# Optimization experiments

Measured on AMD Instinct MI355X. Metric: run time of the kernel, lower is better.

## Reference

```python
import jax, jax.numpy as jnp
import numpy as np

NUM_NODES = 256
IN_FEAT = 64
HIDDEN = 512
N_CLASSES = 2
BATCH = 256


def setup_inputs() -> dict:
    key = jax.random.key(0)
    ks = jax.random.split(key, 10)
    return {
        "z": jax.random.normal(ks[0], (BATCH, 1, NUM_NODES, NUM_NODES), dtype=jnp.float32),
        "node_emb": jax.random.normal(ks[1], (NUM_NODES, IN_FEAT), dtype=jnp.float32),
        "w1": jax.random.normal(ks[2], (IN_FEAT, HIDDEN), dtype=jnp.float32) * (1.0 / np.sqrt(IN_FEAT)),
        "b1": jnp.zeros((HIDDEN,), dtype=jnp.float32),
        "w2": jax.random.normal(ks[3], (HIDDEN, HIDDEN), dtype=jnp.float32) * (1.0 / np.sqrt(HIDDEN)),
        "b2": jnp.zeros((HIDDEN,), dtype=jnp.float32),
        "w3": jax.random.normal(ks[4], (HIDDEN, HIDDEN), dtype=jnp.float32) * (1.0 / np.sqrt(HIDDEN)),
        "b3": jnp.zeros((HIDDEN,), dtype=jnp.float32),
        "fcw": jax.random.normal(ks[5], (HIDDEN, N_CLASSES), dtype=jnp.float32) * (1.0 / np.sqrt(HIDDEN)),
        "fcb": jnp.zeros((N_CLASSES,), dtype=jnp.float32),
    }


def reference(z, node_emb, w1, b1, w2, b2, w3, b3, fcw, fcb):
    # z: (B, 1, N, N) latent interpreted as weighted adjacency
    z_sq = jnp.squeeze(z, axis=1)                         # (B, N, N)
    A = jax.nn.sigmoid(z_sq)
    A = (A + jnp.swapaxes(A, 1, 2)) * 0.5                  # symmetrize
    A_hat = A + jnp.eye(A.shape[-1], dtype=A.dtype)[None]  # add self loops
    D_hat = jnp.sum(A_hat, axis=2) + 1e-6                  # (B, N) degrees
    d_inv_sqrt = D_hat ** -0.5
    # norm_A = D^{-1/2} A_hat D^{-1/2} via row/col scaling (same math as diag bmm)
    norm_A = A_hat * d_inv_sqrt[:, :, None] * d_inv_sqrt[:, None, :]

    X = jnp.broadcast_to(node_emb[None], (z.shape[0],) + node_emb.shape)  # (B, N, F)
    H1 = jax.nn.relu(jnp.einsum('bij,bjh->bih', norm_A, X @ w1 + b1))
    H2 = jax.nn.relu(jnp.einsum('bij,bjh->bih', norm_A, H1 @ w2 + b2))
    H3 = jax.nn.relu(jnp.einsum('bij,bjh->bih', norm_A, H2 @ w3 + b3))
    graph_emb = jnp.mean(H3, axis=1)                       # (B, H)
    logits = graph_emb @ fcw + fcb                         # (B, n_classes)
    return logits
```

## Files before the change

### kernel.cpp

```cpp
#include <hip/hip_runtime.h>
#include <stdint.h>

#define B_ 256
#define N_ 256
#define F_ 64
#define H_ 512

typedef _Float16 f16;
typedef _Float16 f16x8 __attribute__((ext_vector_type(8)));
typedef _Float16 f16x4 __attribute__((ext_vector_type(4)));
typedef _Float16 f16x2 __attribute__((ext_vector_type(2)));
typedef float    f32x4 __attribute__((ext_vector_type(4)));

__device__ __forceinline__ float sigmoidf_(float x) {
    return 1.0f / (1.0f + __expf(-x));
}

#define BAR_ACQ(N) do { \
    asm volatile("s_waitcnt vmcnt(" #N ")" ::: "memory"); \
    __builtin_amdgcn_s_barrier(); \
    __builtin_amdgcn_sched_barrier(0); } while (0)
#define BAR_REL() do { \
    __builtin_amdgcn_sched_barrier(0); \
    __builtin_amdgcn_s_barrier(); } while (0)

__global__ __launch_bounds__(512) void k_fsum(const float* __restrict__ z,
                                              f16* __restrict__ nA) {
    constexpr int LD = 258;
    __shared__ f16 T[256 * LD];
    __shared__ float cpart[8][256];
    __shared__ float rbuf[256];
    __shared__ float Dv[256];

    const int b = blockIdx.x;
    const int tid = threadIdx.x, lane = tid & 63, w = tid >> 6;
    const float* zb = z + (size_t)b * (N_ * N_);

    float colacc[4] = {0.f, 0.f, 0.f, 0.f};
    for (int r = 0; r < 32; r++) {
        int i = w * 32 + r;
        float4 v = *(const float4*)(zb + (size_t)i * N_ + lane * 4);
        float s0 = sigmoidf_(v.x), s1 = sigmoidf_(v.y),
              s2 = sigmoidf_(v.z), s3 = sigmoidf_(v.w);
        f16x2 p0 = { (f16)s0, (f16)s1 }, p1 = { (f16)s2, (f16)s3 };
        *(f16x2*)&T[i * LD + lane * 4]     = p0;
        *(f16x2*)&T[i * LD + lane * 4 + 2] = p1;
        colacc[0] += s0; colacc[1] += s1; colacc[2] += s2; colacc[3] += s3;
        float rs = s0 + s1 + s2 + s3;
        for (int off = 32; off; off >>= 1) rs += __shfl_down(rs, off, 64);
        if (lane == 0) rbuf[i] = rs;
    }
    #pragma unroll
    for (int k = 0; k < 4; k++) cpart[w][lane * 4 + k] = colacc[k];
    __syncthreads();

    if (tid < 256) {
        float cs = 0.f;
        #pragma unroll
        for (int ww = 0; ww < 8; ww++) cs += cpart[ww][tid];
        Dv[tid] = rsqrtf(1.0f + 1e-6f + 0.5f * (rbuf[tid] + cs));
    }
    __syncthreads();

    const int j8 = (tid & 31) * 8;
    float dj[8];
    #pragma unroll
    for (int k = 0; k < 8; k++) dj[k] = Dv[j8 + k];
    f16* Ob = nA + (size_t)b * (N_ * N_);
    for (int it = 0; it < 16; it++) {
        int i = it * 16 + (tid >> 5);
        float di = Dv[i];
        f16x2 dd[4];
        #pragma unroll
        for (int c = 0; c < 4; c++)
            dd[c] = *(const f16x2*)&T[i * LD + j8 + c * 2];
        f16x8 o;
        #pragma unroll
        for (int k = 0; k < 8; k++) {
            float sij = (float)dd[k >> 1][k & 1];
            float v = 0.5f * (sij + (float)T[(j8 + k) * LD + i]);
            if (i == j8 + k) v += 1.0f;
            o[k] = (f16)(v * di * dj[k]);
        }
        *(f16x8*)&Ob[(size_t)i * N_ + j8] = o;
    }
}

__global__ __launch_bounds__(256) void k_prep(const float* __restrict__ ne,
                                              const float* __restrict__ w1,
                                              const float* __restrict__ b1,
                                              const float* __restrict__ w2,
                                              const float* __restrict__ w3,
                                              f16* __restrict__ XW1t,
                                              f16* __restrict__ w2t,
                                              f16* __restrict__ w3t) {
    int bid = blockIdx.x;
    if (bid < 512) {
        int h = bid, node = threadIdx.x;
        float s = b1[h];
        #pragma unroll 8
        for (int k = 0; k < F_; k++) s += ne[node * F_ + k] * w1[k * H_ + h];
        XW1t[h * N_ + node] = (f16)s;
    } else {
        int idx4 = bid - 512;
        int which = idx4 >> 10;
        const float* src = which ? w3 : w2;
        f16* dst = which ? w3t : w2t;
        int idx = (idx4 & 1023) * 256 + threadIdx.x;
        int k = idx >> 9, n = idx & 511;
        dst[n * H_ + k] = (f16)src[k * H_ + n];
    }
}

template <int KDIM, int MODE>
__global__ __launch_bounds__(256, 4) void k_gemm(const f16* __restrict__ A, long aBatch,
                                                 const f16* __restrict__ Bt, long bBatch,
                                                 f16* __restrict__ Out,
                                                 const float* __restrict__ bias,
                                                 float* __restrict__ gp) {
    __shared__ f16 As[128 * 64];
    __shared__ f16 Bs[128 * 64];
    const int tid  = threadIdx.x;
    const int lane = tid & 63, wave = tid >> 6;
    const int wm = wave >> 1, wn = wave & 1;

    const int lin = blockIdx.x;
    const int xcd = lin & 7, q = lin >> 3;
    const int n_t = q & 3, p = q >> 2;
    const int grp = xcd * 64 + p;
    const int b   = grp >> 1, m_t = grp & 1;
    const int m0 = m_t * 128, n0 = n_t * 128;

    const f16* Ab = A + (size_t)b * aBatch;
    const f16* Bb = Bt + (size_t)b * bBatch;

    f32x4 acc[4][4];
    #pragma unroll
    for (int i = 0; i < 4; i++)
        #pragma unroll
        for (int j = 0; j < 4; j++)
            #pragma unroll
            for (int r = 0; r < 4; r++) acc[i][j][r] = 0.0f;

    const int lr = lane >> 3;
    const int kc = (lane & 7) ^ lr;

    const int ln15 = lane & 15;

    for (int kk = 0; kk < KDIM; kk += 64) {
        #pragma unroll
        for (int c = 0; c < 4; c++) {
            int chunk = wave * 4 + c;
            int row = chunk * 8 + lr;
            __builtin_amdgcn_global_load_lds(
                (__attribute__((address_space(1))) void*)(Ab + (size_t)(m0 + row) * KDIM + kk + kc * 8),
                (__attribute__((address_space(3))) void*)(&As[chunk * 512]), 16, 0, 0);
            __builtin_amdgcn_global_load_lds(
                (__attribute__((address_space(1))) void*)(Bb + (size_t)(n0 + row) * KDIM + kk + kc * 8),
                (__attribute__((address_space(3))) void*)(&Bs[chunk * 512]), 16, 0, 0);
        }
        __syncthreads();

        #pragma unroll
        for (int ks = 0; ks < 2; ks++) {
            const int rkc = ks * 4 + (lane >> 4);
            f16x8 aF[4];
            #pragma unroll
            for (int t = 0; t < 4; t++) {
                int ra = wm * 64 + t * 16 + ln15;
                aF[t] = *(const f16x8*)&As[(ra * 8 + (rkc ^ (ra & 7))) * 8];
            }
            #pragma unroll
            for (int h2 = 0; h2 < 2; h2++) {
                f16x8 bF[2];
                #pragma unroll
                for (int t = 0; t < 2; t++) {
                    int rb = wn * 64 + (h2 * 2 + t) * 16 + ln15;
                    bF[t] = *(const f16x8*)&Bs[(rb * 8 + (rkc ^ (rb & 7))) * 8];
                }
                #pragma unroll
                for (int mt = 0; mt < 4; mt++)
                    #pragma unroll
                    for (int t = 0; t < 2; t++)
                        acc[mt][h2 * 2 + t] = __builtin_amdgcn_mfma_f32_16x16x32_f16(aF[mt], bF[t], acc[mt][h2 * 2 + t], 0, 0, 0);
            }
        }
        __syncthreads();
    }

    const int quad = lane >> 4;
    if (MODE == 0) {
        f16* Ob = Out + (size_t)b * (N_ * H_);
        #pragma unroll
        for (int mt = 0; mt < 4; mt++) {
            int node = m0 + wm * 64 + mt * 16 + quad * 4;
            #pragma unroll
            for (int nt = 0; nt < 4; nt++) {
                int h = n0 + wn * 64 + nt * 16 + ln15;
                #pragma unroll
                for (int rr = 0; rr < 4; rr++) {
                    float v = acc[mt][nt][rr];
                    v = v > 0.f ? v : 0.f;
                    Ob[(size_t)(node + rr) * H_ + h] = (f16)v;
                }
            }
        }
    }
}

template <int REDUCE>
__global__ __launch_bounds__(512, 2) void k_fused(const f16* __restrict__ Hin,
                                                  const f16* __restrict__ Wt,
                                                  const float* __restrict__ bias,
                                                  const f16* __restrict__ nA,
                                                  f16* __restrict__ Hout,
                                                  float* __restrict__ gp) {
    __shared__ f16 As[2][16384];
    __shared__ f16 WU[32768];

    const int tid  = threadIdx.x;
    const int lane = tid & 63, wave = tid >> 6;
    const int ln15 = lane & 15, quad = lane >> 4;
    const int wm = wave >> 1, wn = wave & 1;

    const int lin = blockIdx.x;
    const int xcd = lin & 7, p = lin >> 3;
    const int grp = xcd * 128 + p;
    const int b = grp >> 2, hc = grp & 3;

    const f16* Hb = Hin + (size_t)b * (N_ * H_);
    const f16* Ab = nA + (size_t)b * (N_ * N_);
    const f16* Wc = Wt + (size_t)(hc * 128) * H_;

    const int lr = lane >> 3;
    const int kc = (lane & 7) ^ lr;

    auto stage1 = [&](int buf, int kt) {
        #pragma unroll
        for (int c = 0; c < 4; c++) {
            int chunk = wave * 4 + c;
            int row = chunk * 8 + lr;
            __builtin_amdgcn_global_load_lds(
                (__attribute__((address_space(1))) void*)(Hb + (size_t)row * H_ + kt * 64 + kc * 8),
                (__attribute__((address_space(3))) void*)(&As[buf][chunk * 512]), 16, 0, 0);
        }
        #pragma unroll
        for (int c = 0; c < 2; c++) {
            int chunk = wave * 2 + c;
            int row = chunk * 8 + lr;
            __builtin_amdgcn_global_load_lds(
                (__attribute__((address_space(1))) void*)(Wc + (size_t)row * H_ + kt * 64 + kc * 8),
                (__attribute__((address_space(3))) void*)(&WU[buf * 8192 + chunk * 512]), 16, 0, 0);
        }
    };
    auto stage2 = [&](int buf, int jt) {
        #pragma unroll
        for (int c = 0; c < 4; c++) {
            int chunk = wave * 4 + c;
            int row = chunk * 8 + lr;
            __builtin_amdgcn_global_load_lds(
                (__attribute__((address_space(1))) void*)(Ab + (size_t)row * N_ + jt * 64 + kc * 8),
                (__attribute__((address_space(3))) void*)(&As[buf][chunk * 512]), 16, 0, 0);
        }
    };

    f32x4 acc[4][4];
    #pragma unroll
    for (int i = 0; i < 4; i++)
        #pragma unroll
        for (int j = 0; j < 4; j++)
            #pragma unroll
            for (int r = 0; r < 4; r++) acc[i][j][r] = 0.0f;

    stage1(0, 0);
    for (int kt = 0; kt < 8; ++kt) {
        const int buf = kt & 1;
        if (kt < 7) {
            stage1(buf ^ 1, kt + 1);
            BAR_ACQ(6);
        } else {
            stage2(0, 0);
            BAR_ACQ(4);
        }
        __builtin_amdgcn_s_setprio(1);
        #pragma unroll
        for (int ks = 0; ks < 2; ks++) {
            const int rkc = ks * 4 + quad;
            f16x8 aF[4], bF[4];
            #pragma unroll
            for (int t = 0; t < 4; t++) {
                int ra = wm * 64 + t * 16 + ln15;
                aF[t] = *(const f16x8*)&As[buf][(ra * 8 + (rkc ^ (ra & 7))) * 8];
            }
            #pragma unroll
            for (int t = 0; t < 4; t++) {
                int rb = wn * 64 + t * 16 + ln15;
                bF[t] = *(const f16x8*)&WU[buf * 8192 + (rb * 8 + (rkc ^ (rb & 7))) * 8];
            }
            #pragma unroll
            for (int mt = 0; mt < 4; mt++)
                #pragma unroll
                for (int nt = 0; nt < 4; nt++)
                    acc[mt][nt] = __builtin_amdgcn_mfma_f32_16x16x32_f16(aF[mt], bF[nt], acc[mt][nt], 0, 0, 0);
        }
        __builtin_amdgcn_s_setprio(0);
        BAR_REL();
    }

    #pragma unroll
    for (int nt = 0; nt < 4; nt++) {
        int hl = wn * 64 + nt * 16 + ln15;
        float bv = bias[hc * 128 + hl];
        #pragma unroll
        for (int mt = 0; mt < 4; mt++) {
            int j = wm * 64 + mt * 16 + quad * 4;
            int slot = (j >> 3) ^ (hl & 7);
            f16x4 v;
            #pragma unroll
            for (int rr = 0; rr < 4; rr++) v[rr] = (f16)(acc[mt][nt][rr] + bv);
            *(f16x4*)&WU[hl * 256 + slot * 8 + (j & 7)] = v;
        }
    }
    asm volatile("s_waitcnt lgkmcnt(0)" ::: "memory");
    __builtin_amdgcn_s_barrier();
    __builtin_amdgcn_sched_barrier(0);

    #pragma unroll
    for (int i = 0; i < 4; i++)
        #pragma unroll
        for (int j = 0; j < 4; j++)
            #pragma unroll
            for (int r = 0; r < 4; r++) acc[i][j][r] = 0.0f;

    for (int jt = 0; jt < 4; ++jt) {
        const int buf = jt & 1;
        if (jt < 3) {
            stage2(buf ^ 1, jt + 1);
            BAR_ACQ(4);
        } else {
            BAR_ACQ(0);
        }
        __builtin_amdgcn_s_setprio(1);
        #pragma unroll
        for (int ks = 0; ks < 2; ks++) {
            const int rkc = ks * 4 + quad;
            f16x8 aF[4], bF[4];
            #pragma unroll
            for (int t = 0; t < 4; t++) {
                int ra = wm * 64 + t * 16 + ln15;
                aF[t] = *(const f16x8*)&As[buf][(ra * 8 + (rkc ^ (ra & 7))) * 8];
            }
            #pragma unroll
            for (int t = 0; t < 4; t++) {
                int rb = wn * 64 + t * 16 + ln15;
                int g = jt * 8 + rkc;
                bF[t] = *(const f16x8*)&WU[rb * 256 + ((g ^ (rb & 7)) * 8)];
            }
            #pragma unroll
            for (int mt = 0; mt < 4; mt++)
                #pragma unroll
                for (int nt = 0; nt < 4; nt++)
                    acc[mt][nt] = __builtin_amdgcn_mfma_f32_16x16x32_f16(aF[mt], bF[nt], acc[mt][nt], 0, 0, 0);
        }
        __builtin_amdgcn_s_setprio(0);
        BAR_REL();
    }

    if (REDUCE == 0) {
        f16* Ob = Hout + (size_t)b * (N_ * H_);
        #pragma unroll
        for (int mt = 0; mt < 4; mt++) {
            int node = wm * 64 + mt * 16 + quad * 4;
            #pragma unroll
            for (int nt = 0; nt < 4; nt++) {
                int hg = hc * 128 + wn * 64 + nt * 16 + ln15;
                #pragma unroll
                for (int rr = 0; rr < 4; rr++) {
                    float v = acc[mt][nt][rr];
                    v = v > 0.f ? v : 0.f;
                    Ob[(size_t)(node + rr) * H_ + hg] = (f16)v;
                }
            }
        }
    } else {
        float part[4];
        #pragma unroll
        for (int nt = 0; nt < 4; nt++) {
            float s = 0.f;
            #pragma unroll
            for (int mt = 0; mt < 4; mt++)
                #pragma unroll
                for (int rr = 0; rr < 4; rr++) {
                    float v = acc[mt][nt][rr];
                    s += (v > 0.f ? v : 0.f);
                }
            s += __shfl_down(s, 32, 64);
            s += __shfl_down(s, 16, 64);
            part[nt] = s;
        }
        __syncthreads();
        float* red = (float*)&As[0][0];
        if (quad == 0) {
            #pragma unroll
            for (int nt = 0; nt < 4; nt++)
                red[wave * 64 + nt * 16 + ln15] = part[nt];
        }
        __syncthreads();
        if (tid < 128) {
            int wnl = tid >> 6, cl = tid & 63;
            float g = red[(0 * 2 + wnl) * 64 + cl] + red[(1 * 2 + wnl) * 64 + cl]
                    + red[(2 * 2 + wnl) * 64 + cl] + red[(3 * 2 + wnl) * 64 + cl];
            gp[(size_t)b * H_ + hc * 128 + tid] = g;
        }
    }
}

__global__ __launch_bounds__(256) void k_logits(const float* __restrict__ gp,
                                                const float* __restrict__ fcw,
                                                const float* __restrict__ fcb,
                                                float* __restrict__ out) {
    int b = blockIdx.x, tid = threadIdx.x;
    const float* g = gp + (size_t)b * H_;
    float g0 = g[tid];
    float g1 = g[tid + 256];
    float p0 = g0 * fcw[tid * 2 + 0] + g1 * fcw[(tid + 256) * 2 + 0];
    float p1 = g0 * fcw[tid * 2 + 1] + g1 * fcw[(tid + 256) * 2 + 1];
    for (int off = 32; off; off >>= 1) {
        p0 += __shfl_down(p0, off, 64);
        p1 += __shfl_down(p1, off, 64);
    }
    __shared__ float r0[4], r1[4];
    int lane = tid & 63, w = tid >> 6;
    if (lane == 0) { r0[w] = p0; r1[w] = p1; }
    __syncthreads();
    const float inv = 1.0f / N_;
    if (tid == 0) out[b * 2 + 0] = (r0[0] + r0[1] + r0[2] + r0[3]) * inv + fcb[0];
    if (tid == 1) out[b * 2 + 1] = (r1[0] + r1[1] + r1[2] + r1[3]) * inv + fcb[1];
}

extern "C" void kernel_launch(void* const* d_in, const int* in_sizes, int n_in,
                              void* d_out, int out_size, void* d_ws, size_t ws_size,
                              hipStream_t stream) {
    const float* z   = (const float*)d_in[0];
    const float* ne  = (const float*)d_in[1];
    const float* w1  = (const float*)d_in[2];
    const float* b1  = (const float*)d_in[3];
    const float* w2  = (const float*)d_in[4];
    const float* b2  = (const float*)d_in[5];
    const float* w3  = (const float*)d_in[6];
    const float* b3  = (const float*)d_in[7];
    const float* fcw = (const float*)d_in[8];
    const float* fcb = (const float*)d_in[9];
    float* out = (float*)d_out;

    char* ws = (char*)d_ws;
    f16*   T     = (f16*)(ws + 0);
    f16*   nA    = (f16*)(ws + 67108864);
    f16*   Hh    = (f16*)(ws + 100663296);
    float* gpart = (float*)(ws + 100663296);
    f16*   XW1t  = (f16*)(ws + 167772160);
    f16*   w2t   = (f16*)(ws + 168034304);
    f16*   w3t   = (f16*)(ws + 168558592);

    k_fsum<<<256, 512, 0, stream>>>(z, nA);
    k_prep<<<2560, 256, 0, stream>>>(ne, w1, b1, w2, w3, XW1t, w2t, w3t);

    k_gemm<256, 0><<<2048, 256, 0, stream>>>(nA, 65536, XW1t, 0, Hh, nullptr, nullptr);
    k_fused<0><<<1024, 512, 0, stream>>>(Hh, w2t, b2, nA, T, nullptr);
    k_fused<1><<<1024, 512, 0, stream>>>(T, w3t, b3, nA, nullptr, gpart);

    k_logits<<<B_, 256, 0, stream>>>(gpart, fcw, fcb, out);
}
```

Baseline: 308.0 us.

## Swizzle shared sigmoid tile and symmetrize via 8x8 register tiles

Replaces the padded LDS tile with an XOR-swizzled 256x256 half layout written in 8-byte chunks. The symmetrize/normalize pass now loads 8x8 blocks of rows and columns as vector reads and transposes them in registers, instead of doing scalar strided transposed reads. Row sums move from per-row wave shuffles to a separate LDS pass after the barrier. This is meant to cut LDS bank conflicts and the count of LDS instructions in the adjacency-normalization kernel, in exchange for more register pressure and an extra barrier.

```diff
diff --git a/kernel.cpp b/kernel.cpp
--- a/kernel.cpp
+++ b/kernel.cpp
@@ -26,63 +26,86 @@
 
 __global__ __launch_bounds__(512) void k_fsum(const float* __restrict__ z,
                                               f16* __restrict__ nA) {
-    constexpr int LD = 258;
-    __shared__ f16 T[256 * LD];
+    __shared__ f16 T[256 * 256];
     __shared__ float cpart[8][256];
-    __shared__ float rbuf[256];
+    __shared__ float rpart[256][2];
     __shared__ float Dv[256];
 
     const int b = blockIdx.x;
     const int tid = threadIdx.x, lane = tid & 63, w = tid >> 6;
     const float* zb = z + (size_t)b * (N_ * N_);
 
+    auto swz = [](int i) { return (i & 31) ^ (i >> 5); };
+
     float colacc[4] = {0.f, 0.f, 0.f, 0.f};
+    const int ch = lane >> 1, half = lane & 1;
     for (int r = 0; r < 32; r++) {
         int i = w * 32 + r;
         float4 v = *(const float4*)(zb + (size_t)i * N_ + lane * 4);
         float s0 = sigmoidf_(v.x), s1 = sigmoidf_(v.y),
               s2 = sigmoidf_(v.z), s3 = sigmoidf_(v.w);
-        f16x2 p0 = { (f16)s0, (f16)s1 }, p1 = { (f16)s2, (f16)s3 };
-        *(f16x2*)&T[i * LD + lane * 4]     = p0;
-        *(f16x2*)&T[i * LD + lane * 4 + 2] = p1;
+        f16x4 sv = { (f16)s0, (f16)s1, (f16)s2, (f16)s3 };
+        *(f16x4*)&T[i * 256 + ((ch ^ swz(i)) << 3) + half * 4] = sv;
         colacc[0] += s0; colacc[1] += s1; colacc[2] += s2; colacc[3] += s3;
-        float rs = s0 + s1 + s2 + s3;
-        for (int off = 32; off; off >>= 1) rs += __shfl_down(rs, off, 64);
-        if (lane == 0) rbuf[i] = rs;
     }
     #pragma unroll
     for (int k = 0; k < 4; k++) cpart[w][lane * 4 + k] = colacc[k];
     __syncthreads();
 
+    {
+        int i = tid >> 1, h = tid & 1;
+        float s = 0.f;
+        #pragma unroll
+        for (int c = 0; c < 16; c++) {
+            int cc = h * 16 + c;
+            f16x8 v = *(const f16x8*)&T[i * 256 + ((cc ^ swz(i)) << 3)];
+            #pragma unroll
+            for (int k = 0; k < 8; k++) s += (float)v[k];
+        }
+        rpart[i][h] = s;
+    }
+    __syncthreads();
+
     if (tid < 256) {
         float cs = 0.f;
         #pragma unroll
         for (int ww = 0; ww < 8; ww++) cs += cpart[ww][tid];
-        Dv[tid] = rsqrtf(1.0f + 1e-6f + 0.5f * (rbuf[tid] + cs));
+        float rs = rpart[tid][0] + rpart[tid][1];
+        Dv[tid] = rsqrtf(1.0f + 1e-6f + 0.5f * (rs + cs));
     }
     __syncthreads();
 
-    const int j8 = (tid & 31) * 8;
-    float dj[8];
-    #pragma unroll
-    for (int k = 0; k < 8; k++) dj[k] = Dv[j8 + k];
     f16* Ob = nA + (size_t)b * (N_ * N_);
-    for (int it = 0; it < 16; it++) {
-        int i = it * 16 + (tid >> 5);
-        float di = Dv[i];
-        f16x2 dd[4];
-        #pragma unroll
-        for (int c = 0; c < 4; c++)
-            dd[c] = *(const f16x2*)&T[i * LD + j8 + c * 2];
-        f16x8 o;
-        #pragma unroll
-        for (int k = 0; k < 8; k++) {
-            float sij = (float)dd[k >> 1][k & 1];
-            float v = 0.5f * (sij + (float)T[(j8 + k) * LD + i]);
-            if (i == j8 + k) v += 1.0f;
-            o[k] = (f16)(v * di * dj[k]);
-        }
-        *(f16x8*)&Ob[(size_t)i * N_ + j8] = o;
+    #pragma unroll
+    for (int tt = 0; tt < 2; tt++) {
+        int tile = tt * 512 + tid;
+        int I = tile >> 5, J = tile & 31;
+        f16x8 a[8], bm[8];
+        #pragma unroll
+        for (int r = 0; r < 8; r++) {
+            int ia = I * 8 + r;
+            a[r] = *(const f16x8*)&T[ia * 256 + ((J ^ swz(ia)) << 3)];
+        }
+        #pragma unroll
+        for (int r = 0; r < 8; r++) {
+            int jb = J * 8 + r;
+            bm[r] = *(const f16x8*)&T[jb * 256 + ((I ^ swz(jb)) << 3)];
+        }
+        float dj[8];
+        #pragma unroll
+        for (int k = 0; k < 8; k++) dj[k] = Dv[J * 8 + k];
+        #pragma unroll
+        for (int r = 0; r < 8; r++) {
+            float di = Dv[I * 8 + r];
+            f16x8 o;
+            #pragma unroll
+            for (int k = 0; k < 8; k++) {
+                float v = 0.5f * ((float)a[r][k] + (float)bm[k][r]);
+                if (I * 8 + r == J * 8 + k) v += 1.0f;
+                o[k] = (f16)(v * di * dj[k]);
+            }
+            *(f16x8*)&Ob[(size_t)(I * 8 + r) * N_ + J * 8] = o;
+        }
     }
 }
 
```

Result: faster. 298.8 us (-3.0%).
